# Kernel optimization log

Measured on AMD Instinct MI355X. Metric: run time of the kernel, lower is better.

## Reference

```python
import jax, jax.numpy as jnp
import numpy as np

B, N, C_IN, C_OUT, E_DIM = 16, 1024, 64, 64, 4


def setup_inputs() -> dict:
    key = jax.random.key(0)
    ks = jax.random.split(key, 7)
    x = jax.random.normal(ks[0], (B, N, C_IN), dtype=jnp.float32)
    adj = jax.random.uniform(ks[1], (B, N, N), dtype=jnp.float32)
    edge_attr = jax.random.randint(ks[2], (B, N, N, 1), 0, E_DIM, dtype=jnp.int32)
    scale = 1.0 / np.sqrt(C_IN)
    W_rel = jax.random.normal(ks[3], (C_IN, C_OUT), dtype=jnp.float32) * scale
    b_rel = jax.random.normal(ks[4], (C_OUT,), dtype=jnp.float32) * scale
    W_root = jax.random.normal(ks[5], (C_IN, C_OUT), dtype=jnp.float32) * scale
    w_edge = jax.random.normal(ks[6], (E_DIM,), dtype=jnp.float32)
    return {"x": x, "adj": adj, "edge_attr": edge_attr,
            "W_rel": W_rel, "b_rel": b_rel, "W_root": W_root, "w_edge": w_edge}


def reference(x, adj, edge_attr, W_rel, b_rel, W_root, w_edge):
    # one_hot(edge_attr) @ w_edge == gather of w_edge by edge type (same math,
    # avoids materializing the B x N x N x E_DIM one-hot tensor).
    e = w_edge[edge_attr[..., 0]]            # [B, N, N]
    adj_w = adj * e                           # weighted adjacency
    out = jnp.matmul(adj_w, x)                # [B, N, C_IN] aggregation (aggr='add')
    out = jnp.matmul(out, W_rel) + b_rel      # lin_rel
    out = out + jnp.matmul(x, W_root)         # lin_root (no bias)
    return out
```

## Files before the change

### kernel.cpp

```cpp
#include <hip/hip_runtime.h>

#define BB 16
#define NN 1024
#define CC 64

typedef __attribute__((ext_vector_type(8))) short short8;
typedef __attribute__((ext_vector_type(4))) float f32x4;
typedef __attribute__((ext_vector_type(4))) int   i32x4;

typedef __attribute__((address_space(3))) void lds_void_t;
typedef const __attribute__((address_space(1))) void gbl_void_t;

__device__ __forceinline__ void load_lds16(const void* g, void* l) {
    __builtin_amdgcn_global_load_lds((gbl_void_t*)g, (lds_void_t*)l, 16, 0, 0);
}

__device__ __forceinline__ unsigned short bf16_rne(float f) {
    unsigned u = __float_as_uint(f);
    u += 0x7fffu + ((u >> 16) & 1u);
    return (unsigned short)(u >> 16);
}

extern "C" __global__ __launch_bounds__(256)
void precompute(const float* __restrict__ x, const float* __restrict__ W_rel,
                const float* __restrict__ W_root, const float* __restrict__ b_rel,
                unsigned short* __restrict__ xw_sw, float* __restrict__ out)
{
    __shared__ float wrel_s[64 * 64];
    __shared__ float wroot_s[64 * 64];
    __shared__ float x_s[16 * 68];

    const int t = threadIdx.x;
    #pragma unroll
    for (int k = 0; k < 4; ++k) {
        int i4 = t + 256 * k;
        ((float4*)wrel_s)[i4]  = ((const float4*)W_rel)[i4];
        ((float4*)wroot_s)[i4] = ((const float4*)W_root)[i4];
    }
    const int row0 = blockIdx.x * 16;
    {
        int r = t >> 4, c4 = t & 15;
        *(float4*)(x_s + r * 68 + c4 * 4) = ((const float4*)(x + (size_t)(row0 + r) * CC))[c4];
    }
    __syncthreads();

    const int c4 = t & 15;
    const int r  = t >> 4;
    float aw0 = 0.f, aw1 = 0.f, aw2 = 0.f, aw3 = 0.f;
    float ar0 = 0.f, ar1 = 0.f, ar2 = 0.f, ar3 = 0.f;
    const float* xrow = x_s + r * 68;
    #pragma unroll 8
    for (int k = 0; k < 64; ++k) {
        float xv = xrow[k];
        float4 wv = ((const float4*)(wrel_s  + k * 64))[c4];
        float4 rv = ((const float4*)(wroot_s + k * 64))[c4];
        aw0 += xv * wv.x; aw1 += xv * wv.y; aw2 += xv * wv.z; aw3 += xv * wv.w;
        ar0 += xv * rv.x; ar1 += xv * rv.y; ar2 += xv * rv.z; ar3 += xv * rv.w;
    }

    const int row_g = row0 + r;
    {
        const float4 bv = ((const float4*)b_rel)[c4];
        ((float4*)out)[(size_t)row_g * 16 + c4] =
            make_float4(ar0 + bv.x, ar1 + bv.y, ar2 + bv.z, ar3 + bv.w);
    }
    {
        const int b = row_g >> 10;
        const int k = row_g & 1023;
        const int kb = k >> 5;
        const int qk = (k >> 3) & 3;
        const int j  = k & 7;
        const int c  = 4 * c4;
        const int n0 = c >> 4;
        const int n  = c & 15;
        size_t off = ((size_t)b << 16) + (size_t)((kb * 4 + n0) << 9)
                   + (size_t)((n + (qk << 4)) << 3) + j;
        xw_sw[off]      = bf16_rne(aw0);
        xw_sw[off + 8]  = bf16_rne(aw1);
        xw_sw[off + 16] = bf16_rne(aw2);
        xw_sw[off + 24] = bf16_rne(aw3);
    }
}

#define ADJ_OFF 0
#define EA_OFF  16384
#define XW_OFF  32768

extern "C" __global__ __launch_bounds__(256, 3)
void gnn_mfma(const float* __restrict__ adj, const int* __restrict__ ea,
              const float* __restrict__ w_edge,
              const unsigned short* __restrict__ xw_sw,
              float* __restrict__ out)
{
    __shared__ __align__(16) char lds[49152];

    const int t    = threadIdx.x;
    const int w    = t >> 6;
    const int lane = t & 63;
    const int m    = lane & 15;
    const int q    = lane >> 4;
    const int wm   = w >> 1;
    const int wk   = w & 1;

    const int mtile = blockIdx.x & 31;
    const int kh    = (blockIdx.x >> 5) & 1;
    const int b     = blockIdx.x >> 6;
    const int row0  = mtile << 5;

    const float w0 = w_edge[0], w1 = w_edge[1], w2 = w_edge[2], w3 = w_edge[3];
    const float d1 = w1 - w0;
    const float d2 = w2 - 2.f * w1 + w0;
    const float d3 = w3 - 3.f * w2 + 3.f * w1 - w0;
    const float c3 = d3 * (1.f / 6.f);
    const float c2 = 0.5f * d2 - 0.5f * d3;
    const float c1 = d1 - 0.5f * d2 + (1.f / 3.f) * d3;
    const float c0 = w0;

    const size_t bbase = ((size_t)b << 20);
    const unsigned short* xwb = xw_sw + ((size_t)b << 16);

    f32x4 acc0 = {0.f, 0.f, 0.f, 0.f};
    f32x4 acc1 = acc0, acc2 = acc0, acc3 = acc0;

    for (int c = 0; c < 4; ++c) {
        const int kc = (kh << 9) + (c << 7);
        if (c) __syncthreads();

        #pragma unroll
        for (int f = w; f < 16; f += 4) {
            int mh = f >> 3;
            int kb = (f >> 1) & 3;
            int h  = f & 1;
            int row = row0 + (mh << 4) + m;
            int k   = kc + (kb << 5) + (q << 3) + (h << 2);
            size_t goff = bbase + ((size_t)row << 10) + k;
            int doff = ((mh * 4 + kb) << 11) + (h << 10);
            load_lds16(adj + goff, lds + ADJ_OFF + doff);
            load_lds16(ea  + goff, lds + EA_OFF  + doff);
        }
        #pragma unroll
        for (int f = w; f < 16; f += 4) {
            int kb = f >> 2, n0 = f & 3;
            int kbg = (kh << 4) + (c << 2) + kb;
            load_lds16(xwb + (((kbg << 2) + n0) << 9) + (lane << 3),
                       lds + XW_OFF + (f << 10));
        }
        __syncthreads();

        #pragma unroll
        for (int s = 0; s < 2; ++s) {
            int kb = (wk << 1) + s;
            int fbase = ((wm * 4 + kb) << 11) + (lane << 4);
            f32x4 alo = *(const f32x4*)(lds + ADJ_OFF + fbase);
            f32x4 ahi = *(const f32x4*)(lds + ADJ_OFF + fbase + 1024);
            i32x4 elo = *(const i32x4*)(lds + EA_OFF + fbase);
            i32x4 ehi = *(const i32x4*)(lds + EA_OFF + fbase + 1024);

            #define WSEL(ev) __builtin_fmaf(__builtin_fmaf(__builtin_fmaf(c3, (float)(ev), c2), (float)(ev), c1), (float)(ev), c0)
            float p0 = alo[0] * WSEL(elo[0]);
            float p1 = alo[1] * WSEL(elo[1]);
            float p2 = alo[2] * WSEL(elo[2]);
            float p3 = alo[3] * WSEL(elo[3]);
            float p4 = ahi[0] * WSEL(ehi[0]);
            float p5 = ahi[1] * WSEL(ehi[1]);
            float p6 = ahi[2] * WSEL(ehi[2]);
            float p7 = ahi[3] * WSEL(ehi[3]);
            #undef WSEL

            union { int i[4]; short8 s8; } af;
            af.i[0] = __builtin_amdgcn_perm(__float_as_uint(p1), __float_as_uint(p0), 0x07060302u);
            af.i[1] = __builtin_amdgcn_perm(__float_as_uint(p3), __float_as_uint(p2), 0x07060302u);
            af.i[2] = __builtin_amdgcn_perm(__float_as_uint(p5), __float_as_uint(p4), 0x07060302u);
            af.i[3] = __builtin_amdgcn_perm(__float_as_uint(p7), __float_as_uint(p6), 0x07060302u);

            const char* xbase = lds + XW_OFF + ((kb << 2) << 10) + (lane << 4);
            short8 bf0 = *(const short8*)(xbase);
            short8 bf1 = *(const short8*)(xbase + 1024);
            short8 bf2 = *(const short8*)(xbase + 2048);
            short8 bf3 = *(const short8*)(xbase + 3072);

            acc0 = __builtin_amdgcn_mfma_f32_16x16x32_bf16(af.s8, bf0, acc0, 0, 0, 0);
            acc1 = __builtin_amdgcn_mfma_f32_16x16x32_bf16(af.s8, bf1, acc1, 0, 0, 0);
            acc2 = __builtin_amdgcn_mfma_f32_16x16x32_bf16(af.s8, bf2, acc2, 0, 0, 0);
            acc3 = __builtin_amdgcn_mfma_f32_16x16x32_bf16(af.s8, bf3, acc3, 0, 0, 0);
        }
    }

    __syncthreads();
    float* scratch = (float*)lds;
    if (wk == 1) {
        float* buf = scratch + wm * 1088;
        #pragma unroll
        for (int rg = 0; rg < 4; ++rg) {
            int rbase = (q * 4 + rg) * 68 + m;
            buf[rbase]      = acc0[rg];
            buf[rbase + 16] = acc1[rg];
            buf[rbase + 32] = acc2[rg];
            buf[rbase + 48] = acc3[rg];
        }
    }
    __syncthreads();
    if (wk == 0) {
        const float* buf = scratch + wm * 1088;
        float* obase = out + (((size_t)b << 10) + row0 + (wm << 4)) * 64;
        #pragma unroll
        for (int rg = 0; rg < 4; ++rg) {
            int rpad = (q * 4 + rg) * 68 + m;
            int rout = (q * 4 + rg) * 64 + m;
            #pragma unroll
            for (int n0 = 0; n0 < 4; ++n0) {
                float v = (n0 == 0 ? acc0[rg] : n0 == 1 ? acc1[rg] : n0 == 2 ? acc2[rg] : acc3[rg]);
                v += buf[rpad + n0 * 16];
                atomicAdd(obase + rout + n0 * 16, v);
            }
        }
    }
}

extern "C" void kernel_launch(void* const* d_in, const int* in_sizes, int n_in,
                              void* d_out, int out_size, void* d_ws, size_t ws_size,
                              hipStream_t stream) {
    const float* x      = (const float*)d_in[0];
    const float* adj    = (const float*)d_in[1];
    const int*   ea     = (const int*)  d_in[2];
    const float* W_rel  = (const float*)d_in[3];
    const float* b_rel  = (const float*)d_in[4];
    const float* W_root = (const float*)d_in[5];
    const float* w_edge = (const float*)d_in[6];
    float* out = (float*)d_out;

    unsigned short* xw_sw = (unsigned short*)d_ws;

    precompute<<<BB * NN / 16, 256, 0, stream>>>(x, W_rel, W_root, b_rel, xw_sw, out);
    gnn_mfma<<<BB * (NN / 32) * 2, 256, 0, stream>>>(adj, ea, w_edge, xw_sw, out);
}
```

Measured before the change: 171.0 us.

## Pipeline adj/ea staging with triple-buffered LDS and split waves along N

Restructures the main kernel so each wave owns a 16-row by 32-column output slice. Warps now split along N instead of K, which removes the cross-wave LDS reduction. The 128-wide K chunks with full barriers are replaced by 16 steps of 32-wide K, using a triple-buffered LDS ring for adj/edge_attr and double-buffered xw fragments read straight from global into registers. A manual vmcnt wait plus a bare s_barrier overlap the next stage's loads with the current MFMA work. LDS use drops to 24 KB to allow 4 blocks per CU, at the cost of each wave redundantly computing the weighted A fragment and of relying on hand-written waitcnt correctness.

```diff
diff --git a/kernel.cpp b/kernel.cpp
--- a/kernel.cpp
+++ b/kernel.cpp
@@ -82,17 +82,13 @@
     }
 }
 
-#define ADJ_OFF 0
-#define EA_OFF  16384
-#define XW_OFF  32768
-
-extern "C" __global__ __launch_bounds__(256, 3)
+extern "C" __global__ __launch_bounds__(256, 4)
 void gnn_mfma(const float* __restrict__ adj, const int* __restrict__ ea,
               const float* __restrict__ w_edge,
               const unsigned short* __restrict__ xw_sw,
               float* __restrict__ out)
 {
-    __shared__ __align__(16) char lds[49152];
+    __shared__ __align__(16) char lds[24576];
 
     const int t    = threadIdx.x;
     const int w    = t >> 6;
@@ -100,7 +96,7 @@
     const int m    = lane & 15;
     const int q    = lane >> 4;
     const int wm   = w >> 1;
-    const int wk   = w & 1;
+    const int wn   = w & 1;
 
     const int mtile = blockIdx.x & 31;
     const int kh    = (blockIdx.x >> 5) & 1;
@@ -117,103 +113,81 @@
     const float c0 = w0;
 
     const size_t bbase = ((size_t)b << 20);
-    const unsigned short* xwb = xw_sw + ((size_t)b << 16);
+    const int row_s = row0 + (wm << 4) + m;
+    const int kbase = (kh << 9) + (q << 3) + (wn << 2);
+    const float* adjp = adj + bbase + ((size_t)row_s << 10) + kbase;
+    const int*   eap  = ea  + bbase + ((size_t)row_s << 10) + kbase;
+    const int dA = (wm << 11) + (wn << 10);
+
+    const unsigned short* xwp = xw_sw + ((size_t)b << 16)
+                              + ((size_t)(((kh << 4) << 2) + (wn << 1)) << 9)
+                              + ((size_t)lane << 3);
 
     f32x4 acc0 = {0.f, 0.f, 0.f, 0.f};
-    f32x4 acc1 = acc0, acc2 = acc0, acc3 = acc0;
-
-    for (int c = 0; c < 4; ++c) {
-        const int kc = (kh << 9) + (c << 7);
-        if (c) __syncthreads();
-
-        #pragma unroll
-        for (int f = w; f < 16; f += 4) {
-            int mh = f >> 3;
-            int kb = (f >> 1) & 3;
-            int h  = f & 1;
-            int row = row0 + (mh << 4) + m;
-            int k   = kc + (kb << 5) + (q << 3) + (h << 2);
-            size_t goff = bbase + ((size_t)row << 10) + k;
-            int doff = ((mh * 4 + kb) << 11) + (h << 10);
-            load_lds16(adj + goff, lds + ADJ_OFF + doff);
-            load_lds16(ea  + goff, lds + EA_OFF  + doff);
+    f32x4 acc1 = acc0;
+    short8 bfr[2][2];
+
+#define WSEL(ev) __builtin_fmaf(__builtin_fmaf(__builtin_fmaf(c3, (float)(ev), c2), (float)(ev), c1), (float)(ev), c0)
+#define BUFP(i) (lds + 8192 * (i))
+#define STAGE(c, bi) do { \
+        load_lds16(adjp + ((c) << 5), BUFP(bi) + dA); \
+        load_lds16(eap  + ((c) << 5), BUFP(bi) + 4096 + dA); \
+    } while (0)
+#define LDBF(c, r) do { \
+        bfr[r][0] = *(const short8*)(xwp + ((size_t)(c) << 11)); \
+        bfr[r][1] = *(const short8*)(xwp + ((size_t)(c) << 11) + 512); \
+    } while (0)
+#define COMPUTE(bi, r) do { \
+        const char* fb = BUFP(bi) + (wm << 11) + (lane << 4); \
+        f32x4 alo = *(const f32x4*)(fb); \
+        f32x4 ahi = *(const f32x4*)(fb + 1024); \
+        i32x4 elo = *(const i32x4*)(fb + 4096); \
+        i32x4 ehi = *(const i32x4*)(fb + 5120); \
+        float p0 = alo[0] * WSEL(elo[0]); \
+        float p1 = alo[1] * WSEL(elo[1]); \
+        float p2 = alo[2] * WSEL(elo[2]); \
+        float p3 = alo[3] * WSEL(elo[3]); \
+        float p4 = ahi[0] * WSEL(ehi[0]); \
+        float p5 = ahi[1] * WSEL(ehi[1]); \
+        float p6 = ahi[2] * WSEL(ehi[2]); \
+        float p7 = ahi[3] * WSEL(ehi[3]); \
+        union { int i[4]; short8 s8; } af; \
+        af.i[0] = __builtin_amdgcn_perm(__float_as_uint(p1), __float_as_uint(p0), 0x07060302u); \
+        af.i[1] = __builtin_amdgcn_perm(__float_as_uint(p3), __float_as_uint(p2), 0x07060302u); \
+        af.i[2] = __builtin_amdgcn_perm(__float_as_uint(p5), __float_as_uint(p4), 0x07060302u); \
+        af.i[3] = __builtin_amdgcn_perm(__float_as_uint(p7), __float_as_uint(p6), 0x07060302u); \
+        acc0 = __builtin_amdgcn_mfma_f32_16x16x32_bf16(af.s8, bfr[r][0], acc0, 0, 0, 0); \
+        acc1 = __builtin_amdgcn_mfma_f32_16x16x32_bf16(af.s8, bfr[r][1], acc1, 0, 0, 0); \
+    } while (0)
+
+    STAGE(0, 0);
+    LDBF(0, 0);
+
+    #pragma unroll 16
+    for (int c = 0; c < 16; ++c) {
+        if (c < 15) {
+            STAGE(c + 1, (c + 1) % 3);
+            LDBF(c + 1, (c + 1) & 1);
+            asm volatile("s_waitcnt vmcnt(4)" ::: "memory");
+        } else {
+            asm volatile("s_waitcnt vmcnt(0)" ::: "memory");
         }
-        #pragma unroll
-        for (int f = w; f < 16; f += 4) {
-            int kb = f >> 2, n0 = f & 3;
-            int kbg = (kh << 4) + (c << 2) + kb;
-            load_lds16(xwb + (((kbg << 2) + n0) << 9) + (lane << 3),
-                       lds + XW_OFF + (f << 10));
-        }
-        __syncthreads();
-
-        #pragma unroll
-        for (int s = 0; s < 2; ++s) {
-            int kb = (wk << 1) + s;
-            int fbase = ((wm * 4 + kb) << 11) + (lane << 4);
-            f32x4 alo = *(const f32x4*)(lds + ADJ_OFF + fbase);
-            f32x4 ahi = *(const f32x4*)(lds + ADJ_OFF + fbase + 1024);
-            i32x4 elo = *(const i32x4*)(lds + EA_OFF + fbase);
-            i32x4 ehi = *(const i32x4*)(lds + EA_OFF + fbase + 1024);
-
-            #define WSEL(ev) __builtin_fmaf(__builtin_fmaf(__builtin_fmaf(c3, (float)(ev), c2), (float)(ev), c1), (float)(ev), c0)
-            float p0 = alo[0] * WSEL(elo[0]);
-            float p1 = alo[1] * WSEL(elo[1]);
-            float p2 = alo[2] * WSEL(elo[2]);
-            float p3 = alo[3] * WSEL(elo[3]);
-            float p4 = ahi[0] * WSEL(ehi[0]);
-            float p5 = ahi[1] * WSEL(ehi[1]);
-            float p6 = ahi[2] * WSEL(ehi[2]);
-            float p7 = ahi[3] * WSEL(ehi[3]);
-            #undef WSEL
-
-            union { int i[4]; short8 s8; } af;
-            af.i[0] = __builtin_amdgcn_perm(__float_as_uint(p1), __float_as_uint(p0), 0x07060302u);
-            af.i[1] = __builtin_amdgcn_perm(__float_as_uint(p3), __float_as_uint(p2), 0x07060302u);
-            af.i[2] = __builtin_amdgcn_perm(__float_as_uint(p5), __float_as_uint(p4), 0x07060302u);
-            af.i[3] = __builtin_amdgcn_perm(__float_as_uint(p7), __float_as_uint(p6), 0x07060302u);
-
-            const char* xbase = lds + XW_OFF + ((kb << 2) << 10) + (lane << 4);
-            short8 bf0 = *(const short8*)(xbase);
-            short8 bf1 = *(const short8*)(xbase + 1024);
-            short8 bf2 = *(const short8*)(xbase + 2048);
-            short8 bf3 = *(const short8*)(xbase + 3072);
-
-            acc0 = __builtin_amdgcn_mfma_f32_16x16x32_bf16(af.s8, bf0, acc0, 0, 0, 0);
-            acc1 = __builtin_amdgcn_mfma_f32_16x16x32_bf16(af.s8, bf1, acc1, 0, 0, 0);
-            acc2 = __builtin_amdgcn_mfma_f32_16x16x32_bf16(af.s8, bf2, acc2, 0, 0, 0);
-            acc3 = __builtin_amdgcn_mfma_f32_16x16x32_bf16(af.s8, bf3, acc3, 0, 0, 0);
-        }
-    }
-
-    __syncthreads();
-    float* scratch = (float*)lds;
-    if (wk == 1) {
-        float* buf = scratch + wm * 1088;
-        #pragma unroll
-        for (int rg = 0; rg < 4; ++rg) {
-            int rbase = (q * 4 + rg) * 68 + m;
-            buf[rbase]      = acc0[rg];
-            buf[rbase + 16] = acc1[rg];
-            buf[rbase + 32] = acc2[rg];
-            buf[rbase + 48] = acc3[rg];
-        }
-    }
-    __syncthreads();
-    if (wk == 0) {
-        const float* buf = scratch + wm * 1088;
-        float* obase = out + (((size_t)b << 10) + row0 + (wm << 4)) * 64;
-        #pragma unroll
-        for (int rg = 0; rg < 4; ++rg) {
-            int rpad = (q * 4 + rg) * 68 + m;
-            int rout = (q * 4 + rg) * 64 + m;
-            #pragma unroll
-            for (int n0 = 0; n0 < 4; ++n0) {
-                float v = (n0 == 0 ? acc0[rg] : n0 == 1 ? acc1[rg] : n0 == 2 ? acc2[rg] : acc3[rg]);
-                v += buf[rpad + n0 * 16];
-                atomicAdd(obase + rout + n0 * 16, v);
-            }
-        }
+        __builtin_amdgcn_s_barrier();
+        COMPUTE(c % 3, c & 1);
+    }
+
+#undef COMPUTE
+#undef LDBF
+#undef STAGE
+#undef BUFP
+#undef WSEL
+
+    float* ob = out + ((((size_t)b << 10) + row0 + (wm << 4) + (q << 2)) << 6)
+              + (wn << 5) + m;
+    #pragma unroll
+    for (int rg = 0; rg < 4; ++rg) {
+        atomicAdd(ob + rg * 64,      acc0[rg]);
+        atomicAdd(ob + rg * 64 + 16, acc1[rg]);
     }
 }
 
```

Measured after the change: 171.8 us. About the same (+0.5%).
